# Optimization experiments

Hardware: AMD Instinct MI355X
Metric: run time of the kernel (lower is better)

## Reference

```python
import jax, jax.numpy as jnp
import numpy as np

B, T, F, H = 256, 128, 32, 1024  # batch, seq_len(=decoder steps), input/output feat, hidden


def lstm_cell(x, h, c, Wih, Whh, b):
    # PyTorch gate order: i, f, g, o
    gates = x @ Wih.T + h @ Whh.T + b  # [B, 4H]
    i, f, g, o = jnp.split(gates, 4, axis=-1)
    i, f, o = jax.nn.sigmoid(i), jax.nn.sigmoid(f), jax.nn.sigmoid(o)
    c_new = f * c + i * jnp.tanh(g)
    h_new = o * jnp.tanh(c_new)
    return h_new, c_new


def setup_inputs() -> dict:
    key = jax.random.key(0)
    ks = jax.random.split(key, 16)
    s = 0.05
    d = {
        "input_seq": jax.random.normal(ks[0], (B, T, F), jnp.float32),
        # encoder LSTM (2 layers); bias = bias_ih + bias_hh folded together
        "enc_Wih0": jax.random.normal(ks[1], (4 * H, F), jnp.float32) * s,
        "enc_Whh0": jax.random.normal(ks[2], (4 * H, H), jnp.float32) * s,
        "enc_b0": jax.random.normal(ks[3], (4 * H,), jnp.float32) * s,
        "enc_Wih1": jax.random.normal(ks[4], (4 * H, H), jnp.float32) * s,
        "enc_Whh1": jax.random.normal(ks[5], (4 * H, H), jnp.float32) * s,
        "enc_b1": jax.random.normal(ks[6], (4 * H,), jnp.float32) * s,
        # decoder LSTM (2 layers), input size = output_size = F
        "dec_Wih0": jax.random.normal(ks[7], (4 * H, F), jnp.float32) * s,
        "dec_Whh0": jax.random.normal(ks[8], (4 * H, H), jnp.float32) * s,
        "dec_b0": jax.random.normal(ks[9], (4 * H,), jnp.float32) * s,
        "dec_Wih1": jax.random.normal(ks[10], (4 * H, H), jnp.float32) * s,
        "dec_Whh1": jax.random.normal(ks[11], (4 * H, H), jnp.float32) * s,
        "dec_b1": jax.random.normal(ks[12], (4 * H,), jnp.float32) * s,
        # output head
        "lin_W": jax.random.normal(ks[13], (F, H), jnp.float32) * s,
        "lin_b": jax.random.normal(ks[14], (F,), jnp.float32) * s,
    }
    return d


def reference(input_seq, enc_Wih0, enc_Whh0, enc_b0, enc_Wih1, enc_Whh1, enc_b1,
              dec_Wih0, dec_Whh0, dec_b0, dec_Wih1, dec_Whh1, dec_b1, lin_W, lin_b):
    Bsz = input_seq.shape[0]
    zeros = jnp.zeros((Bsz, H), input_seq.dtype)

    # ---- encoder: 2-layer LSTM scanned over time ----
    def enc_step(carry, x_t):
        h0, c0, h1, c1 = carry
        h0, c0 = lstm_cell(x_t, h0, c0, enc_Wih0, enc_Whh0, enc_b0)
        h1, c1 = lstm_cell(h0, h1, c1, enc_Wih1, enc_Whh1, enc_b1)
        return (h0, c0, h1, c1), None

    xs = jnp.swapaxes(input_seq, 0, 1)  # [T, B, F]
    (h0, c0, h1, c1), _ = jax.lax.scan(enc_step, (zeros, zeros, zeros, zeros), xs)

    def dec_step(carry, _):
        x, h0, c0, h1, c1 = carry
        h0, c0 = lstm_cell(x, h0, c0, dec_Wih0, dec_Whh0, dec_b0)
        h1, c1 = lstm_cell(h0, h1, c1, dec_Wih1, dec_Whh1, dec_b1)
        out = h1 @ lin_W.T + lin_b  # [B, F]
        return (out, h0, c0, h1, c1), out

    dec_in0 = input_seq[:, -1, :]  # [B, F]
    _, outs = jax.lax.scan(dec_step, (dec_in0, h0, c0, h1, c1), None, length=T)
    return jnp.swapaxes(outs, 0, 1)  # [B, T, F]
```

## Files before the change

### kernel.cpp

```cpp
#include <hip/hip_runtime.h>

typedef _Float16 half_t;
typedef _Float16 half8 __attribute__((ext_vector_type(8)));
typedef _Float16 half4v __attribute__((ext_vector_type(4)));
typedef float f32x4 __attribute__((ext_vector_type(4)));

#define DI __device__ __forceinline__

constexpr int Bsz = 256;
constexpr int Tsz = 128;
constexpr int Fsz = 32;
constexpr int Hsz = 1024;
constexpr int NG  = 4096;
constexpr int K1  = 1152;
constexpr int K2  = 2048;
constexpr int RSTR = 84;
constexpr int RING = 32;
constexpr int OBR  = 32;
constexpr int SZA  = Bsz * K1;
constexpr int SLOT = Bsz * Hsz;
constexpr int NPH  = 256 + 3 * Tsz;

DI int perm_to_orig(int np) {
    int nt = np >> 6, r = np & 63, g = r >> 4, jo = r & 15;
    return g * Hsz + nt * 16 + jo;
}

DI size_t wfrag(int np, int k) {
    return ((size_t)((k >> 5) * 256 + (np >> 4)) * 64 + ((k >> 3) & 3) * 16 + (np & 15)) * 8 + (k & 7);
}
DI size_t afrag(int b, int k) {
    return ((size_t)((k >> 5) * 16 + (b >> 4)) * 64 + ((k >> 3) & 3) * 16 + (b & 15)) * 8 + (k & 7);
}
DI size_t lfrag(int f, int k) {
    return ((size_t)((k >> 5) * 2 + (f >> 4)) * 64 + ((k >> 3) & 3) * 16 + (f & 15)) * 8 + (k & 7);
}

DI void store8_wt(half_t* p, half4v v) {
    unsigned long long bits;
    __builtin_memcpy(&bits, &v, 8);
    __hip_atomic_store((unsigned long long*)p, bits, __ATOMIC_RELAXED, __HIP_MEMORY_SCOPE_AGENT);
}
DI void store4_wt(half_t* p, half_t a, half_t b) {
    half_t t2[2] = {a, b};
    unsigned bits;
    __builtin_memcpy(&bits, t2, 4);
    __hip_atomic_store((unsigned*)p, bits, __ATOMIC_RELAXED, __HIP_MEMORY_SCOPE_AGENT);
}


__global__ void pack_cat(half_t* __restrict__ dst, const float* __restrict__ srcA, int KA,
                         const float* __restrict__ srcB, int KB, int KP) {
    int tid = threadIdx.x;
    int np = blockIdx.y * 64 + (tid & 63);
    int k0 = (blockIdx.x * 4 + (tid >> 6)) * 8;
    if (k0 >= KP) return;
    int n = perm_to_orig(np);
    half8 v;
#pragma unroll
    for (int j = 0; j < 8; ++j) {
        int k = k0 + j;
        float f = 0.f;
        if (k < KA) f = srcA[(size_t)n * KA + k];
        else if (k < KA + KB) f = srcB[(size_t)n * KB + (k - KA)];
        v[j] = (half_t)f;
    }
    *(half8*)(dst + wfrag(np, k0)) = v;
}

__global__ void pack_small(half_t* __restrict__ linWp, half_t* __restrict__ slot0,
                           half_t* __restrict__ obufL,
                           const float* __restrict__ linW, const float* __restrict__ inseq) {
    int idx = blockIdx.x * 256 + threadIdx.x;
    if (idx < 32 * (Hsz / 8)) {
        int f = idx & 31, k0 = (idx >> 5) * 8;
        half8 v;
#pragma unroll
        for (int j = 0; j < 8; ++j) v[j] = (half_t)linW[(size_t)f * Hsz + k0 + j];
        *(half8*)(linWp + lfrag(f, k0)) = v;
    }
    if (idx < Bsz * 4) {
        int b = idx >> 2, f0 = (idx & 3) * 8;
        half8 v, u;
#pragma unroll
        for (int j = 0; j < 8; ++j) {
            v[j] = (half_t)inseq[(size_t)b * (Tsz * Fsz) + f0 + j];
            u[j] = (half_t)inseq[(size_t)b * (Tsz * Fsz) + (Tsz - 1) * Fsz + f0 + j];
        }
        *(half8*)(slot0 + afrag(b, 1024 + f0)) = v;
        *(half8*)(obufL + (size_t)b * Fsz + f0) = u;
    }
}

__global__ void pack_bias(float* __restrict__ b4, const float* eb0, const float* eb1,
                          const float* db0, const float* db1) {
    int idx = blockIdx.x * 256 + threadIdx.x;
    if (idx >= 4 * NG) return;
    int which = idx >> 12, np = idx & (NG - 1);
    int n = perm_to_orig(np);
    const float* src = which == 0 ? eb0 : which == 1 ? eb1 : which == 2 ? db0 : db1;
    b4[idx] = src[n];
}


struct MegaArgs {
    const float* in_seq;
    const half_t *W0e, *W1e, *W0d, *W1d, *linWp;
    const float *lin_b;
    const float *be1, *be2, *bd1, *bd2;
    float *c0, *c1;
    half_t *RH0, *RH1, *H1h, *obuf;
    float* ybuf;
    unsigned* cnt;
};

DI void group_wait(unsigned* cnt, unsigned tgt, int tid) {
    if (tgt) {
        if (tid == 0) {
            while (__hip_atomic_load(cnt, __ATOMIC_RELAXED, __HIP_MEMORY_SCOPE_AGENT) < tgt)
                __builtin_amdgcn_s_sleep(1);
        }
        __syncthreads();
        asm volatile("" ::: "memory");
        __builtin_amdgcn_sched_barrier(0);
    }
}

template <int K, int XM>
DI void gemm_phase(const half_t* __restrict__ A0, const half_t* __restrict__ A1,
                   const half_t* __restrict__ W, const float* __restrict__ bias,
                   float* __restrict__ c, half_t* __restrict__ hdst,
                   const half_t* __restrict__ xobuf,
                   const float* __restrict__ xsrc, half_t* __restrict__ xdst,
                   int mt, int nt, int tid, unsigned* cnt, unsigned tgt,
                   float (&red)[4][64][RSTR]) {
    constexpr int CHW = (K / 32) / 4;
    int lane = tid & 63, w = tid >> 6;
    int l15 = lane & 15, l4 = lane >> 4;
    const half_t* abase;
    int cb;
    if (K == K1)     { abase = A0; cb = w * CHW; }
    else if (w < 2)  { abase = A0; cb = w * CHW; }
    else             { abase = A1; cb = (w - 2) * CHW; }
    const half_t* pa = abase + ((size_t)(cb * 16 + mt * 4) * 64 + lane) * 8;
    const half_t* pw = W + ((size_t)((w * CHW) * 256 + nt * 4) * 64 + lane) * 8;
    const bool xm3 = (XM == 1) && (w == 3);
    const half_t* pobuf = (XM == 1) ? (xobuf + (size_t)mt * 2048 + l15 * 32 + l4 * 8) : nullptr;

    f32x4 acc[4][4] = {};
    half8 bA[3][4], bW[3][4];

#define LDW(st, kk)                                                                  \
    {                                                                                \
        if (!(XM == 1 && xm3 && (kk) >= 6)) {                                        \
            _Pragma("unroll") for (int ni = 0; ni < 4; ++ni)                         \
                bW[st][ni] = *(const half8*)(pw + (size_t)(kk) * 131072 + ni * 512); \
        }                                                                            \
    }
#define LDA(st, kk)                                                                  \
    {                                                                                \
        if (XM == 1 && xm3 && (kk) == 5) {                                           \
            _Pragma("unroll") for (int mi = 0; mi < 4; ++mi)                         \
                bA[st][mi] = *(const half8*)(pobuf + mi * 512);                      \
        } else if (!(XM == 1 && xm3 && (kk) >= 6)) {                                 \
            _Pragma("unroll") for (int mi = 0; mi < 4; ++mi)                         \
                bA[st][mi] = *(const half8*)(pa + (size_t)(kk) * 8192 + mi * 512);   \
        }                                                                            \
    }

    LDW(0, 0)
    LDW(1, 1)

    group_wait(cnt, tgt, tid);

    LDA(0, 0)
    LDA(1, 1)
#pragma unroll
    for (int kk = 0; kk < CHW; ++kk) {
        if (kk + 2 < CHW) { LDW((kk + 2) % 3, kk + 2) LDA((kk + 2) % 3, kk + 2) }
        const int st = kk % 3;
        if (!(XM == 1 && xm3 && kk >= 6)) {
#pragma unroll
            for (int mi = 0; mi < 4; ++mi)
#pragma unroll
                for (int ni = 0; ni < 4; ++ni)
                    acc[mi][ni] = __builtin_amdgcn_mfma_f32_16x16x32_f16(bA[st][mi], bW[st][ni], acc[mi][ni], 0, 0, 0);
        }
    }
#undef LDW
#undef LDA

#pragma unroll
    for (int mi = 0; mi < 4; ++mi)
#pragma unroll
        for (int ni = 0; ni < 4; ++ni)
#pragma unroll
            for (int r = 0; r < 4; ++r)
                red[w][mi * 16 + l4 * 4 + r][ni * 16 + l15] = acc[mi][ni][r];
    __syncthreads();

    int row = tid >> 2, q = tid & 3, jo0 = q * 4;
    f32x4 g0 = {}, g1 = {}, g2 = {}, g3 = {};
#pragma unroll
    for (int ww = 0; ww < 4; ++ww) {
        g0 += *(const f32x4*)&red[ww][row][jo0];
        g1 += *(const f32x4*)&red[ww][row][16 + jo0];
        g2 += *(const f32x4*)&red[ww][row][32 + jo0];
        g3 += *(const f32x4*)&red[ww][row][48 + jo0];
    }
    const float* bb = bias + nt * 64;
    g0 += *(const f32x4*)(bb + jo0);
    g1 += *(const f32x4*)(bb + 16 + jo0);
    g2 += *(const f32x4*)(bb + 32 + jo0);
    g3 += *(const f32x4*)(bb + 48 + jo0);

    int bglob = mt * 64 + row;
    int jg0 = nt * 16 + jo0;
    float* cp = c + (size_t)bglob * Hsz + jg0;
    f32x4 cold = *(const f32x4*)cp;
    f32x4 cnew;
    half4v hv;
#pragma unroll
    for (int e = 0; e < 4; ++e) {
        float si = 1.f / (1.f + __expf(-g0[e]));
        float sf = 1.f / (1.f + __expf(-g1[e]));
        float tg = 1.f - 2.f / (__expf(2.f * g2[e]) + 1.f);
        float so = 1.f / (1.f + __expf(-g3[e]));
        float cn = sf * cold[e] + si * tg;
        cnew[e] = cn;
        float th = 1.f - 2.f / (__expf(2.f * cn) + 1.f);
        hv[e] = (half_t)(so * th);
    }
    *(f32x4*)cp = cnew;

    store8_wt(hdst + afrag(bglob, jg0), hv);

    if (xsrc && nt == 0) {
        int f0 = q * 8;
        const float* xs = xsrc + (size_t)bglob * (Tsz * Fsz) + f0;
        half_t v[8];
#pragma unroll
        for (int j = 0; j < 8; ++j) v[j] = (half_t)xs[j];
        half4v lo = {v[0], v[1], v[2], v[3]}, hi = {v[4], v[5], v[6], v[7]};
        half_t* xp = xdst + afrag(bglob, 1024 + f0);
        store8_wt(xp, lo);
        store8_wt(xp + 4, hi);
    }
}

DI void out_phase(const half_t* __restrict__ h1, const half_t* __restrict__ lw,
                  const float* __restrict__ lb, float* __restrict__ ybt,
                  half_t* __restrict__ ob,
                  int mt, int nt, int tid, unsigned* cnt, unsigned tgt,
                  float (&red)[4][64][RSTR]) {
    int lane = tid & 63, w = tid >> 6;
    bool worker = (nt < 4);
    int rt = mt * 4 + nt;

    group_wait(cnt, tgt, tid);

    if (worker) {
        const half_t* pa = h1 + ((size_t)((w * 8) * 16 + rt) * 64 + lane) * 8;
        const half_t* pb = lw + ((size_t)(w * 8) * 2 * 64 + lane) * 8;
        f32x4 ac0 = {}, ac1 = {};
#pragma unroll
        for (int kk = 0; kk < 8; ++kk) {
            half8 a = *(const half8*)(pa + (size_t)kk * 8192);
            half8 b0 = *(const half8*)(pb + kk * 1024);
            half8 b1 = *(const half8*)(pb + kk * 1024 + 512);
            ac0 = __builtin_amdgcn_mfma_f32_16x16x32_f16(a, b0, ac0, 0, 0, 0);
            ac1 = __builtin_amdgcn_mfma_f32_16x16x32_f16(a, b1, ac1, 0, 0, 0);
        }
        int l15 = lane & 15, l4 = lane >> 4;
#pragma unroll
        for (int r = 0; r < 4; ++r) {
            red[w][l4 * 4 + r][l15] = ac0[r];
            red[w][l4 * 4 + r][16 + l15] = ac1[r];
        }
    }
    __syncthreads();
    if (worker) {
        int row = tid >> 4;
        int f0 = (tid & 15) * 2;
        float v0 = red[0][row][f0] + red[1][row][f0] + red[2][row][f0] + red[3][row][f0] + lb[f0];
        float v1 = red[0][row][f0 + 1] + red[1][row][f0 + 1] + red[2][row][f0 + 1] + red[3][row][f0 + 1] + lb[f0 + 1];
        int bglob = mt * 64 + nt * 16 + row;
        float* yp = ybt + (size_t)bglob * (Tsz * Fsz);
        yp[f0] = v0;
        yp[f0 + 1] = v1;
        store4_wt(ob + (size_t)bglob * Fsz + f0, (half_t)v0, (half_t)v1);
    }
}

__launch_bounds__(256, 1) __global__ void mega_kernel(MegaArgs g) {
    __shared__ __align__(16) float red[4][64][RSTR];
    int bid = blockIdx.x;
    int low3 = bid & 7, rest = bid >> 3;
    int mt = rest & 3, nt = ((rest >> 2) << 3) | low3;
    int tid = threadIdx.x;
    unsigned* cnt = g.cnt + mt * 64;

#pragma unroll 1
    for (int p = 0; p < NPH; ++p) {
        unsigned tgt = 64u * (unsigned)p;
        if (p < 256) {
            int t = p >> 1;
            if (!(p & 1)) {
                gemm_phase<K1, 0>(g.RH0 + (size_t)(t & (RING - 1)) * SZA, nullptr,
                                  g.W0e, g.be1, g.c0,
                                  g.RH0 + (size_t)((t + 1) & (RING - 1)) * SZA,
                                  nullptr, nullptr, nullptr,
                                  mt, nt, tid, cnt, tgt, red);
            } else {
                int tsel = (t + 1 < Tsz) ? t + 1 : Tsz - 1;
                gemm_phase<K2, 0>(g.RH0 + (size_t)((t + 1) & (RING - 1)) * SZA,
                                  g.RH1 + (size_t)(t & (RING - 1)) * SLOT,
                                  g.W1e, g.be2, g.c1,
                                  g.RH1 + (size_t)((t + 1) & (RING - 1)) * SLOT,
                                  nullptr,
                                  g.in_seq + (size_t)tsel * Fsz,
                                  g.RH0 + (size_t)((t + 1) & (RING - 1)) * SZA,
                                  mt, nt, tid, cnt, tgt, red);
            }
        } else {
            int qq = p - 256;
            int t = qq / 3, r = qq - t * 3;
            if (r == 0) {
                gemm_phase<K1, 1>(g.RH0 + (size_t)((128 + t) & (RING - 1)) * SZA, nullptr,
                                  g.W0d, g.bd1, g.c0,
                                  g.RH0 + (size_t)((128 + t + 1) & (RING - 1)) * SZA,
                                  g.obuf + (size_t)((t + OBR - 1) & (OBR - 1)) * (Bsz * Fsz),
                                  nullptr, nullptr,
                                  mt, nt, tid, cnt, tgt, red);
            } else if (r == 1) {
                gemm_phase<K2, 0>(g.RH0 + (size_t)((128 + t + 1) & (RING - 1)) * SZA,
                                  (t == 0) ? g.RH1 : g.H1h + (size_t)(t - 1) * SLOT,
                                  g.W1d, g.bd2, g.c1,
                                  g.H1h + (size_t)t * SLOT,
                                  nullptr, nullptr, nullptr,
                                  mt, nt, tid, cnt, tgt, red);
            } else {
                out_phase(g.H1h + (size_t)t * SLOT, g.linWp, g.lin_b,
                          g.ybuf + (size_t)t * Fsz,
                          g.obuf + (size_t)(t & (OBR - 1)) * (Bsz * Fsz),
                          mt, nt, tid, cnt, tgt, red);
            }
        }
        __syncthreads();
        if (tid == 0)
            __hip_atomic_fetch_add(cnt, 1u, __ATOMIC_RELAXED, __HIP_MEMORY_SCOPE_AGENT);
    }
}

__global__ void copy_out(const float* __restrict__ src, float* __restrict__ dst) {
    int i = blockIdx.x * 256 + threadIdx.x;
    ((f32x4*)dst)[i] = ((const f32x4*)src)[i];
}


extern "C" void kernel_launch(void* const* d_in, const int* in_sizes, int n_in,
                              void* d_out, int out_size, void* d_ws, size_t ws_size,
                              hipStream_t stream) {
    (void)in_sizes; (void)n_in;
    const float* in_seq = (const float*)d_in[0];
    const float* eWih0 = (const float*)d_in[1];
    const float* eWhh0 = (const float*)d_in[2];
    const float* eb0 = (const float*)d_in[3];
    const float* eWih1 = (const float*)d_in[4];
    const float* eWhh1 = (const float*)d_in[5];
    const float* eb1 = (const float*)d_in[6];
    const float* dWih0 = (const float*)d_in[7];
    const float* dWhh0 = (const float*)d_in[8];
    const float* db0 = (const float*)d_in[9];
    const float* dWih1 = (const float*)d_in[10];
    const float* dWhh1 = (const float*)d_in[11];
    const float* db1 = (const float*)d_in[12];
    const float* linW = (const float*)d_in[13];
    const float* linb = (const float*)d_in[14];
    float* out = (float*)d_out;

    char* base = (char*)d_ws;
    size_t off = 0;
    auto alloc = [&](size_t bytes) {
        char* r = base + off;
        off = (off + bytes + 255) & ~(size_t)255;
        return r;
    };
    half_t* W0e = (half_t*)alloc((size_t)NG * K1 * 2);
    half_t* W1e = (half_t*)alloc((size_t)NG * K2 * 2);
    half_t* W0d = (half_t*)alloc((size_t)NG * K1 * 2);
    half_t* W1d = (half_t*)alloc((size_t)NG * K2 * 2);
    half_t* linWp = (half_t*)alloc((size_t)32 * Hsz * 2);
    float* bias4 = (float*)alloc((size_t)4 * NG * 4);
    float* c0 = (float*)alloc((size_t)Bsz * Hsz * 4);
    float* c1 = (float*)alloc((size_t)Bsz * Hsz * 4);
    half_t* RH0 = (half_t*)alloc((size_t)RING * SZA * 2);
    half_t* RH1 = (half_t*)alloc((size_t)RING * SLOT * 2);
    half_t* H1h = (half_t*)alloc((size_t)Tsz * SLOT * 2);
    half_t* obuf = (half_t*)alloc((size_t)OBR * Bsz * Fsz * 2);
    float* ybuf = (float*)alloc((size_t)Bsz * Tsz * Fsz * 4);
    unsigned* barCnt = (unsigned*)alloc(4 * 64 * sizeof(unsigned));

    if (off > ws_size) {
        hipMemsetAsync(d_out, 0, (size_t)out_size * 4, stream);
        return;
    }

    hipMemsetAsync(c0, 0, (size_t)Bsz * Hsz * 4, stream);
    hipMemsetAsync(c1, 0, (size_t)Bsz * Hsz * 4, stream);
    hipMemsetAsync(RH0, 0, (size_t)RING * SZA * 2, stream);
    hipMemsetAsync(RH1, 0, (size_t)SLOT * 2, stream);
    hipMemsetAsync(barCnt, 0, 4 * 64 * sizeof(unsigned), stream);

    pack_cat<<<dim3(K1 / 32, NG / 64), 256, 0, stream>>>(W0e, eWhh0, 1024, eWih0, 32, K1);
    pack_cat<<<dim3(K2 / 32, NG / 64), 256, 0, stream>>>(W1e, eWih1, 1024, eWhh1, 1024, K2);
    pack_cat<<<dim3(K1 / 32, NG / 64), 256, 0, stream>>>(W0d, dWhh0, 1024, dWih0, 32, K1);
    pack_cat<<<dim3(K2 / 32, NG / 64), 256, 0, stream>>>(W1d, dWih1, 1024, dWhh1, 1024, K2);
    pack_small<<<16, 256, 0, stream>>>(linWp, RH0, obuf + (size_t)(OBR - 1) * (Bsz * Fsz),
                                       linW, in_seq);
    pack_bias<<<(4 * NG + 255) / 256, 256, 0, stream>>>(bias4, eb0, eb1, db0, db1);

    MegaArgs ma;
    ma.in_seq = in_seq;
    ma.W0e = W0e; ma.W1e = W1e; ma.W0d = W0d; ma.W1d = W1d; ma.linWp = linWp;
    ma.lin_b = linb;
    ma.be1 = bias4; ma.be2 = bias4 + NG; ma.bd1 = bias4 + 2 * NG; ma.bd2 = bias4 + 3 * NG;
    ma.c0 = c0; ma.c1 = c1;
    ma.RH0 = RH0; ma.RH1 = RH1; ma.H1h = H1h; ma.obuf = obuf;
    ma.ybuf = ybuf;
    ma.cnt = barCnt;
    void* kargs[] = {&ma};
    hipError_t ce = hipLaunchCooperativeKernel((const void*)mega_kernel, dim3(256), dim3(256),
                                               kargs, 0, stream);
    if (ce != hipSuccess) {
        mega_kernel<<<dim3(256), dim3(256), 0, stream>>>(ma);
    }

    copy_out<<<(Bsz * Tsz * Fsz / 4) / 256, 256, 0, stream>>>(ybuf, out);
}
```

Baseline: 7.884 ms.

## Keep LSTM cell state in LDS and use nontemporal/coherent activation loads

Cell states c0/c1 now live in per-block shared memory, since each block owns a fixed (batch, hidden) tile across all timesteps. This removes the global read and write of c on every phase, along with the workspace allocation and memsets. Activation loads become nontemporal, the obuf feedback load becomes agent-scope atomic (coherent) loads, and the warp-3 K-skip now applies to all K1 phases rather than only the decoder path. This adds LDS usage and changes cache behaviour for the loads, which could affect occupancy and load latency.

```diff
diff --git a/kernel.cpp b/kernel.cpp
--- a/kernel.cpp
+++ b/kernel.cpp
@@ -15,6 +15,7 @@
 constexpr int K1  = 1152;
 constexpr int K2  = 2048;
 constexpr int RSTR = 84;
+constexpr int CSTR = 24;
 constexpr int RING = 32;
 constexpr int OBR  = 32;
 constexpr int SZA  = Bsz * K1;
@@ -46,6 +47,17 @@
     unsigned bits;
     __builtin_memcpy(&bits, t2, 4);
     __hip_atomic_store((unsigned*)p, bits, __ATOMIC_RELAXED, __HIP_MEMORY_SCOPE_AGENT);
+}
+
+DI half8 load16_coh(const half_t* p) {
+    unsigned long long lo = __hip_atomic_load((const unsigned long long*)p,
+                                              __ATOMIC_RELAXED, __HIP_MEMORY_SCOPE_AGENT);
+    unsigned long long hi = __hip_atomic_load((const unsigned long long*)(p + 4),
+                                              __ATOMIC_RELAXED, __HIP_MEMORY_SCOPE_AGENT);
+    unsigned long long arr[2] = {lo, hi};
+    half8 v;
+    __builtin_memcpy(&v, arr, 16);
+    return v;
 }
 
 
@@ -108,7 +120,6 @@
     const half_t *W0e, *W1e, *W0d, *W1d, *linWp;
     const float *lin_b;
     const float *be1, *be2, *bd1, *bd2;
-    float *c0, *c1;
     half_t *RH0, *RH1, *H1h, *obuf;
     float* ybuf;
     unsigned* cnt;
@@ -129,7 +140,7 @@
 template <int K, int XM>
 DI void gemm_phase(const half_t* __restrict__ A0, const half_t* __restrict__ A1,
                    const half_t* __restrict__ W, const float* __restrict__ bias,
-                   float* __restrict__ c, half_t* __restrict__ hdst,
+                   float (&cls)[2][64][CSTR], int ci, half_t* __restrict__ hdst,
                    const half_t* __restrict__ xobuf,
                    const float* __restrict__ xsrc, half_t* __restrict__ xdst,
                    int mt, int nt, int tid, unsigned* cnt, unsigned tgt,
@@ -144,7 +155,7 @@
     else             { abase = A1; cb = (w - 2) * CHW; }
     const half_t* pa = abase + ((size_t)(cb * 16 + mt * 4) * 64 + lane) * 8;
     const half_t* pw = W + ((size_t)((w * CHW) * 256 + nt * 4) * 64 + lane) * 8;
-    const bool xm3 = (XM == 1) && (w == 3);
+    const bool w3k1 = (K == K1) && (w == 3);
     const half_t* pobuf = (XM == 1) ? (xobuf + (size_t)mt * 2048 + l15 * 32 + l4 * 8) : nullptr;
 
     f32x4 acc[4][4] = {};
@@ -152,19 +163,20 @@
 
 #define LDW(st, kk)                                                                  \
     {                                                                                \
-        if (!(XM == 1 && xm3 && (kk) >= 6)) {                                        \
+        if (!(w3k1 && (kk) >= 6)) {                                                  \
             _Pragma("unroll") for (int ni = 0; ni < 4; ++ni)                         \
                 bW[st][ni] = *(const half8*)(pw + (size_t)(kk) * 131072 + ni * 512); \
         }                                                                            \
     }
 #define LDA(st, kk)                                                                  \
     {                                                                                \
-        if (XM == 1 && xm3 && (kk) == 5) {                                           \
+        if (XM == 1 && w3k1 && (kk) == 5) {                                          \
             _Pragma("unroll") for (int mi = 0; mi < 4; ++mi)                         \
-                bA[st][mi] = *(const half8*)(pobuf + mi * 512);                      \
-        } else if (!(XM == 1 && xm3 && (kk) >= 6)) {                                 \
+                bA[st][mi] = load16_coh(pobuf + mi * 512);                           \
+        } else if (!(w3k1 && (kk) >= 6)) {                                           \
             _Pragma("unroll") for (int mi = 0; mi < 4; ++mi)                         \
-                bA[st][mi] = *(const half8*)(pa + (size_t)(kk) * 8192 + mi * 512);   \
+                bA[st][mi] = __builtin_nontemporal_load(                             \
+                    (const half8*)(pa + (size_t)(kk) * 8192 + mi * 512));            \
         }                                                                            \
     }
 
@@ -179,7 +191,7 @@
     for (int kk = 0; kk < CHW; ++kk) {
         if (kk + 2 < CHW) { LDW((kk + 2) % 3, kk + 2) LDA((kk + 2) % 3, kk + 2) }
         const int st = kk % 3;
-        if (!(XM == 1 && xm3 && kk >= 6)) {
+        if (!(w3k1 && kk >= 6)) {
 #pragma unroll
             for (int mi = 0; mi < 4; ++mi)
 #pragma unroll
@@ -216,8 +228,7 @@
 
     int bglob = mt * 64 + row;
     int jg0 = nt * 16 + jo0;
-    float* cp = c + (size_t)bglob * Hsz + jg0;
-    f32x4 cold = *(const f32x4*)cp;
+    f32x4 cold = *(const f32x4*)&cls[ci][row][jo0];
     f32x4 cnew;
     half4v hv;
 #pragma unroll
@@ -231,7 +242,7 @@
         float th = 1.f - 2.f / (__expf(2.f * cn) + 1.f);
         hv[e] = (half_t)(so * th);
     }
-    *(f32x4*)cp = cnew;
+    *(f32x4*)&cls[ci][row][jo0] = cnew;
 
     store8_wt(hdst + afrag(bglob, jg0), hv);
 
@@ -265,7 +276,7 @@
         f32x4 ac0 = {}, ac1 = {};
 #pragma unroll
         for (int kk = 0; kk < 8; ++kk) {
-            half8 a = *(const half8*)(pa + (size_t)kk * 8192);
+            half8 a = __builtin_nontemporal_load((const half8*)(pa + (size_t)kk * 8192));
             half8 b0 = *(const half8*)(pb + kk * 1024);
             half8 b1 = *(const half8*)(pb + kk * 1024 + 512);
             ac0 = __builtin_amdgcn_mfma_f32_16x16x32_f16(a, b0, ac0, 0, 0, 0);
@@ -294,11 +305,15 @@
 
 __launch_bounds__(256, 1) __global__ void mega_kernel(MegaArgs g) {
     __shared__ __align__(16) float red[4][64][RSTR];
+    __shared__ __align__(16) float cls[2][64][CSTR];
     int bid = blockIdx.x;
     int low3 = bid & 7, rest = bid >> 3;
     int mt = rest & 3, nt = ((rest >> 2) << 3) | low3;
     int tid = threadIdx.x;
     unsigned* cnt = g.cnt + mt * 64;
+
+    for (int i = tid; i < 2 * 64 * CSTR; i += 256) ((float*)cls)[i] = 0.f;
+    __syncthreads();
 
 #pragma unroll 1
     for (int p = 0; p < NPH; ++p) {
@@ -307,7 +322,7 @@
             int t = p >> 1;
             if (!(p & 1)) {
                 gemm_phase<K1, 0>(g.RH0 + (size_t)(t & (RING - 1)) * SZA, nullptr,
-                                  g.W0e, g.be1, g.c0,
+                                  g.W0e, g.be1, cls, 0,
                                   g.RH0 + (size_t)((t + 1) & (RING - 1)) * SZA,
                                   nullptr, nullptr, nullptr,
                                   mt, nt, tid, cnt, tgt, red);
@@ -315,7 +330,7 @@
                 int tsel = (t + 1 < Tsz) ? t + 1 : Tsz - 1;
                 gemm_phase<K2, 0>(g.RH0 + (size_t)((t + 1) & (RING - 1)) * SZA,
                                   g.RH1 + (size_t)(t & (RING - 1)) * SLOT,
-                                  g.W1e, g.be2, g.c1,
+                                  g.W1e, g.be2, cls, 1,
                                   g.RH1 + (size_t)((t + 1) & (RING - 1)) * SLOT,
                                   nullptr,
                                   g.in_seq + (size_t)tsel * Fsz,
@@ -327,7 +342,7 @@
             int t = qq / 3, r = qq - t * 3;
             if (r == 0) {
                 gemm_phase<K1, 1>(g.RH0 + (size_t)((128 + t) & (RING - 1)) * SZA, nullptr,
-                                  g.W0d, g.bd1, g.c0,
+                                  g.W0d, g.bd1, cls, 0,
                                   g.RH0 + (size_t)((128 + t + 1) & (RING - 1)) * SZA,
                                   g.obuf + (size_t)((t + OBR - 1) & (OBR - 1)) * (Bsz * Fsz),
                                   nullptr, nullptr,
@@ -335,7 +350,7 @@
             } else if (r == 1) {
                 gemm_phase<K2, 0>(g.RH0 + (size_t)((128 + t + 1) & (RING - 1)) * SZA,
                                   (t == 0) ? g.RH1 : g.H1h + (size_t)(t - 1) * SLOT,
-                                  g.W1d, g.bd2, g.c1,
+                                  g.W1d, g.bd2, cls, 1,
                                   g.H1h + (size_t)t * SLOT,
                                   nullptr, nullptr, nullptr,
                                   mt, nt, tid, cnt, tgt, red);
@@ -392,8 +407,6 @@
     half_t* W1d = (half_t*)alloc((size_t)NG * K2 * 2);
     half_t* linWp = (half_t*)alloc((size_t)32 * Hsz * 2);
     float* bias4 = (float*)alloc((size_t)4 * NG * 4);
-    float* c0 = (float*)alloc((size_t)Bsz * Hsz * 4);
-    float* c1 = (float*)alloc((size_t)Bsz * Hsz * 4);
     half_t* RH0 = (half_t*)alloc((size_t)RING * SZA * 2);
     half_t* RH1 = (half_t*)alloc((size_t)RING * SLOT * 2);
     half_t* H1h = (half_t*)alloc((size_t)Tsz * SLOT * 2);
@@ -406,8 +419,6 @@
         return;
     }
 
-    hipMemsetAsync(c0, 0, (size_t)Bsz * Hsz * 4, stream);
-    hipMemsetAsync(c1, 0, (size_t)Bsz * Hsz * 4, stream);
     hipMemsetAsync(RH0, 0, (size_t)RING * SZA * 2, stream);
     hipMemsetAsync(RH1, 0, (size_t)SLOT * 2, stream);
     hipMemsetAsync(barCnt, 0, 4 * 64 * sizeof(unsigned), stream);
@@ -425,7 +436,6 @@
     ma.W0e = W0e; ma.W1e = W1e; ma.W0d = W0d; ma.W1d = W1d; ma.linWp = linWp;
     ma.lin_b = linb;
     ma.be1 = bias4; ma.be2 = bias4 + NG; ma.bd1 = bias4 + 2 * NG; ma.bd2 = bias4 + 3 * NG;
-    ma.c0 = c0; ma.c1 = c1;
     ma.RH0 = RH0; ma.RH1 = RH1; ma.H1h = H1h; ma.obuf = obuf;
     ma.ybuf = ybuf;
     ma.cnt = barCnt;
```

Result: slower. 10.26 ms (+30.1%).
